# Kernel optimization log

Measured on AMD Instinct MI355X. Metric: run time of the kernel, lower is better.

Reference implementation:

```python
import jax, jax.numpy as jnp
import numpy as np

N, B = 16384, 64
NMC, RF = 4, 512
D0, D1, D2 = 1024, 512, 256
NATT, DATT = 4, 32


def _layer_norm(x, eps=1e-5):
    mu = jnp.mean(x, axis=-1, keepdims=True)
    var = jnp.var(x, axis=-1, keepdims=True)
    return (x - mu) / jnp.sqrt(var + eps)


def _rf_features(z):
    # rbf random features: concat(cos, sin) / sqrt(num_RF)
    scale = 1.0 / np.sqrt(z.shape[-1]).astype(np.float32)
    return jnp.concatenate([jnp.cos(z), jnp.sin(z)], axis=-1) * scale


def setup_inputs() -> dict:
    key = jax.random.key(0)
    ks = jax.random.split(key, 9)
    X = jax.random.normal(ks[0], (N, D0), dtype=jnp.float32)
    X_idx = jnp.sort(jax.random.randint(ks[1], (N,), 0, B, dtype=jnp.int32))
    Omega1 = jax.random.normal(ks[2], (NMC, D0, RF), dtype=jnp.float32) / np.sqrt(D0).astype(np.float32)
    Omega2 = jax.random.normal(ks[3], (NMC, D1, RF), dtype=jnp.float32) / np.sqrt(D1).astype(np.float32)
    W1 = jax.random.normal(ks[4], (2 * RF, D1), dtype=jnp.float32) * 0.02
    b1 = jnp.zeros((D1,), dtype=jnp.float32)
    W2 = jax.random.normal(ks[5], (2 * RF, D2), dtype=jnp.float32) * 0.02
    b2 = jnp.zeros((D2,), dtype=jnp.float32)
    Ws = jax.random.normal(ks[6], (D2, NATT), dtype=jnp.float32) * 0.02
    bs = jnp.zeros((NATT,), dtype=jnp.float32)
    Wm = jax.random.normal(ks[7], (D2, NATT * DATT), dtype=jnp.float32) * 0.02
    bm = jnp.zeros((NATT * DATT,), dtype=jnp.float32)
    return {"X": X, "X_idx": X_idx, "Omega1": Omega1, "Omega2": Omega2,
            "W1": W1, "b1": b1, "W2": W2, "b2": b2,
            "Ws": Ws, "bs": bs, "Wm": Wm, "bm": bm}


def reference(X, X_idx, Omega1, Omega2, W1, b1, W2, b2, Ws, bs, Wm, bm):
    # --- DGP_RF stack: two Omega(RF) + Linear blocks, MC-sampled Omegas ---
    z1 = jnp.einsum('nd,mdr->mnr', X, Omega1)            # [nMC, N, RF]
    phi1 = _layer_norm(_rf_features(z1))                  # [nMC, N, 2RF]
    h1 = jnp.einsum('mnf,fd->mnd', phi1, W1) + b1         # [nMC, N, D1]
    z2 = jnp.einsum('mnd,mdr->mnr', h1, Omega2)           # [nMC, N, RF]
    phi2 = _layer_norm(_rf_features(z2))                  # [nMC, N, 2RF]
    emb = jnp.einsum('mnf,fd->mnd', phi2, W2) + b2        # [nMC, N, D2]

    # --- Seed_Vecs: attention scores, segment softmax over instances ---
    scores = jnp.transpose(jnp.einsum('mnd,dk->mnk', emb, Ws) + bs, (1, 0, 2))  # [N, nMC, nAtt]
    probs = scores / np.sqrt(D2).astype(np.float32)
    seg = jax.ops.segment_sum(jnp.exp(probs), X_idx, num_segments=B)            # [B, nMC, nAtt]
    probs = jnp.exp(probs - jnp.log(seg)[X_idx])                                # segment softmax

    # --- MHa_Transform (default activation relu) + weighted segment pooling ---
    emb_new = jnp.transpose(jax.nn.relu(jnp.einsum('mnd,de->mne', emb, Wm) + bm), (1, 0, 2))  # [N, nMC, nAtt*dAtt]
    probs_rep = jnp.repeat(probs, DATT, axis=2)                                  # [N, nMC, nAtt*dAtt]
    embedds = jax.ops.segment_sum(emb_new * probs_rep, X_idx, num_segments=B)    # [B, nMC, nAtt*dAtt]
    return embedds
```

## Files before the change

kernel.cpp:

```cpp
#include <hip/hip_runtime.h>

#define NTOT 16384
#define NBAG 64
#define NMC  4

typedef __attribute__((ext_vector_type(8))) short bf8_t;
typedef __attribute__((ext_vector_type(4))) float f32x4;
typedef __attribute__((ext_vector_type(8))) unsigned short u16x8;

#define GLD16(g, l) __builtin_amdgcn_global_load_lds( \
    (const __attribute__((address_space(1))) void*)(g), \
    (__attribute__((address_space(3))) void*)(l), 16, 0, 0)

static __device__ __forceinline__ unsigned short f2bf(float x){
  unsigned int u = __float_as_uint(x);
  u += 0x7fffu + ((u >> 16) & 1u);
  return (unsigned short)(u >> 16);
}
static __device__ __forceinline__ float bf2f(unsigned short h){
  return __uint_as_float(((unsigned int)h) << 16);
}
static __device__ __forceinline__ f32x4 mfma16(bf8_t a, bf8_t b, f32x4 c){
  return __builtin_amdgcn_mfma_f32_16x16x32_bf16(a, b, c, 0, 0, 0);
}

__global__ __launch_bounds__(256) void k_cvt(const float* __restrict__ src,
    unsigned short* __restrict__ dst, int n8){
  for (int i = blockIdx.x*256 + threadIdx.x; i < n8; i += gridDim.x*256){
    float4 v0 = ((const float4*)src)[i*2];
    float4 v1 = ((const float4*)src)[i*2+1];
    u16x8 o;
    o[0]=f2bf(v0.x); o[1]=f2bf(v0.y); o[2]=f2bf(v0.z); o[3]=f2bf(v0.w);
    o[4]=f2bf(v1.x); o[5]=f2bf(v1.y); o[6]=f2bf(v1.z); o[7]=f2bf(v1.w);
    ((u16x8*)dst)[i] = o;
  }
}

__global__ __launch_bounds__(256) void k_pack8(const float* __restrict__ src,
    unsigned short* __restrict__ dst, int K, int N){
  const size_t base = (size_t)blockIdx.y * K * N;
  int idx = blockIdx.x*256 + threadIdx.x;
  int kg = idx / N, c = idx % N;
  const float* s = src + base + (size_t)(kg*8)*N + c;
  u16x8 o;
  #pragma unroll
  for (int i=0;i<8;i++) o[i] = f2bf(s[(size_t)i*N]);
  ((u16x8*)(dst + base))[idx] = o;
}

template<int RT>
static __device__ __forceinline__ void rf_ln_store(f32x4 (&acc)[RT][16],
    unsigned short* __restrict__ phiM, float* rowp, int row0,
    int n0, int ch, int l){
  const float scale = 0.044194173824159216f;
  const int g = l >> 4, li = l & 15;
  float part[RT][4];
  #pragma unroll
  for (int rt=0; rt<RT; rt++){
    #pragma unroll
    for (int j=0;j<4;j++){
      float s = 0.f;
      #pragma unroll
      for (int ct=0; ct<16; ct++){
        float sn, cs; __sincosf(acc[rt][ct][j], &sn, &cs);
        s += sn + cs;
      }
      #pragma unroll
      for (int off=1; off<16; off<<=1) s += __shfl_xor(s, off);
      part[rt][j] = s;
    }
  }
  __syncthreads();
  if (li == 0){
    #pragma unroll
    for (int rt=0; rt<RT; rt++)
      #pragma unroll
      for (int j=0;j<4;j++)
        rowp[(row0 + rt*16 + 4*g + j)*2 + ch] = part[rt][j];
  }
  __syncthreads();
  #pragma unroll
  for (int rt=0; rt<RT; rt++){
    #pragma unroll
    for (int j=0;j<4;j++){
      int rb = row0 + rt*16 + 4*g + j;
      float tot = rowp[rb*2+0] + rowp[rb*2+1];
      float mu = tot * (scale / 1024.0f);
      float rs = 1.0f / sqrtf((1.0f/1024.0f) - mu*mu + 1e-5f);
      size_t base = (size_t)(n0 + rb) * 1024;
      #pragma unroll
      for (int ct=0; ct<16; ct++){
        int c = ch*256 + ct*16 + li;
        float sn, cs; __sincosf(acc[rt][ct][j], &sn, &cs);
        phiM[base + c]       = f2bf((cs*scale - mu)*rs);
        phiM[base + 512 + c] = f2bf((sn*scale - mu)*rs);
      }
    }
  }
}


__global__ __launch_bounds__(512,2) void k_phi1(const unsigned short* __restrict__ Xb,
    const unsigned short* __restrict__ Om1f, unsigned short* __restrict__ phi){
  const int m = blockIdx.y, n0 = blockIdx.x*128;
  const int t = threadIdx.x, w = t>>6, l = t&63;
  const int g = l>>4, li = l&15;
  const int wrg = w>>1, ch = w&1;
  const int wvb = (t & ~63);
  __shared__ unsigned short Bs[4][16384];
  __shared__ float rowp[256];
  f32x4 acc[2][16];
  const f32x4 z4 = {0.f,0.f,0.f,0.f};
  #pragma unroll
  for (int rt=0;rt<2;rt++)
    #pragma unroll
    for (int ct=0;ct<16;ct++) acc[rt][ct] = z4;
  const unsigned short* bsrc = Om1f + (size_t)m*524288;
  const unsigned short* ar0 = Xb + (size_t)(n0 + wrg*32 + li)*1024 + g*8;
  const unsigned short* ar1 = ar0 + 16*1024;
  #pragma unroll
  for (int it=0; it<4; it++) GLD16(bsrc + it*4096 + t*8, &Bs[0][0] + it*4096 + wvb*8);
  #pragma unroll
  for (int it=0; it<4; it++) GLD16(bsrc + 16384 + it*4096 + t*8, &Bs[1][0] + it*4096 + wvb*8);
  bf8_t a0c = *(const bf8_t*)(ar0);       bf8_t a1c = *(const bf8_t*)(ar1);
  bf8_t a0n = *(const bf8_t*)(ar0 + 32);  bf8_t a1n = *(const bf8_t*)(ar1 + 32);
  for (int ks=0; ks<32; ks++){
    int ksn = ks+2 < 32 ? ks+2 : 31;
    const unsigned short* sb = bsrc + (size_t)ksn*16384;
    unsigned short* db = &Bs[(ks+2)&3][0];
    #pragma unroll
    for (int it=0; it<4; it++) GLD16(sb + it*4096 + t*8, db + it*4096 + wvb*8);
    bf8_t a0nn = *(const bf8_t*)(ar0 + ksn*32);
    bf8_t a1nn = *(const bf8_t*)(ar1 + ksn*32);
    asm volatile("s_waitcnt vmcnt(12)" ::: "memory");
    __builtin_amdgcn_sched_barrier(0);
    __builtin_amdgcn_s_barrier();
    __builtin_amdgcn_sched_barrier(0);
    const unsigned short* bb = &Bs[ks&3][0] + g*4096 + (ch*256)*8;
    __builtin_amdgcn_s_setprio(1);
    #pragma unroll
    for (int ct=0; ct<16; ct++){
      bf8_t b = *(const bf8_t*)(bb + (ct*16 + li)*8);
      acc[0][ct] = mfma16(a0c, b, acc[0][ct]);
      acc[1][ct] = mfma16(a1c, b, acc[1][ct]);
    }
    __builtin_amdgcn_s_setprio(0);
    a0c=a0n; a1c=a1n; a0n=a0nn; a1n=a1nn;
  }
  rf_ln_store<2>(acc, phi + (size_t)m*NTOT*1024, rowp, wrg*32, n0, ch, l);
}

__global__ __launch_bounds__(512,2) void k_phi2a(const unsigned short* __restrict__ phi,
    const unsigned short* __restrict__ W1f, const float* __restrict__ b1,
    unsigned short* __restrict__ h){
  const int m = blockIdx.y, n0 = blockIdx.x*128;
  const int t = threadIdx.x, w = t>>6, l = t&63;
  const int g = l>>4, li = l&15;
  const int wrg = w>>1, ch = w&1;
  const int wvb = (t & ~63);
  __shared__ unsigned short Bs[4][16384];
  f32x4 acc[2][16];
  const f32x4 z4 = {0.f,0.f,0.f,0.f};
  #pragma unroll
  for (int rt=0;rt<2;rt++)
    #pragma unroll
    for (int ct=0;ct<16;ct++) acc[rt][ct] = z4;
  const unsigned short* ar0 = phi + ((size_t)m*NTOT + n0 + wrg*32 + li)*1024 + g*8;
  const unsigned short* ar1 = ar0 + 16*1024;
  #pragma unroll
  for (int it=0; it<4; it++) GLD16(W1f + it*4096 + t*8, &Bs[0][0] + it*4096 + wvb*8);
  #pragma unroll
  for (int it=0; it<4; it++) GLD16(W1f + 16384 + it*4096 + t*8, &Bs[1][0] + it*4096 + wvb*8);
  bf8_t a0c = *(const bf8_t*)(ar0);       bf8_t a1c = *(const bf8_t*)(ar1);
  bf8_t a0n = *(const bf8_t*)(ar0 + 32);  bf8_t a1n = *(const bf8_t*)(ar1 + 32);
  for (int ks=0; ks<32; ks++){
    int ksn = ks+2 < 32 ? ks+2 : 31;
    const unsigned short* sb = W1f + (size_t)ksn*16384;
    unsigned short* db = &Bs[(ks+2)&3][0];
    #pragma unroll
    for (int it=0; it<4; it++) GLD16(sb + it*4096 + t*8, db + it*4096 + wvb*8);
    bf8_t a0nn = *(const bf8_t*)(ar0 + ksn*32);
    bf8_t a1nn = *(const bf8_t*)(ar1 + ksn*32);
    asm volatile("s_waitcnt vmcnt(12)" ::: "memory");
    __builtin_amdgcn_sched_barrier(0);
    __builtin_amdgcn_s_barrier();
    __builtin_amdgcn_sched_barrier(0);
    const unsigned short* bb = &Bs[ks&3][0] + g*4096 + (ch*256)*8;
    __builtin_amdgcn_s_setprio(1);
    #pragma unroll
    for (int ct=0; ct<16; ct++){
      bf8_t b = *(const bf8_t*)(bb + (ct*16 + li)*8);
      acc[0][ct] = mfma16(a0c, b, acc[0][ct]);
      acc[1][ct] = mfma16(a1c, b, acc[1][ct]);
    }
    __builtin_amdgcn_s_setprio(0);
    a0c=a0n; a1c=a1n; a0n=a0nn; a1n=a1nn;
  }
  #pragma unroll
  for (int rt=0; rt<2; rt++){
    #pragma unroll
    for (int ct=0; ct<16; ct++){
      int c = ch*256 + ct*16 + li;
      float bv = b1[c];
      #pragma unroll
      for (int j=0;j<4;j++)
        h[((size_t)m*NTOT + n0 + wrg*32 + rt*16 + 4*g + j)*512 + c] = f2bf(acc[rt][ct][j] + bv);
    }
  }
}

__global__ __launch_bounds__(512,2) void k_phi2b(const unsigned short* __restrict__ h,
    const unsigned short* __restrict__ Om2f, unsigned short* __restrict__ phi){
  const int m = blockIdx.y, n0 = blockIdx.x*128;
  const int t = threadIdx.x, w = t>>6, l = t&63;
  const int g = l>>4, li = l&15;
  const int wrg = w>>1, ch = w&1;
  const int wvb = (t & ~63);
  __shared__ unsigned short Bs[4][16384];
  __shared__ float rowp[256];
  f32x4 acc[2][16];
  const f32x4 z4 = {0.f,0.f,0.f,0.f};
  #pragma unroll
  for (int rt=0;rt<2;rt++)
    #pragma unroll
    for (int ct=0;ct<16;ct++) acc[rt][ct] = z4;
  const unsigned short* bsrc = Om2f + (size_t)m*262144;
  const unsigned short* ar0 = h + ((size_t)m*NTOT + n0 + wrg*32 + li)*512 + g*8;
  const unsigned short* ar1 = ar0 + 16*512;
  #pragma unroll
  for (int it=0; it<4; it++) GLD16(bsrc + it*4096 + t*8, &Bs[0][0] + it*4096 + wvb*8);
  #pragma unroll
  for (int it=0; it<4; it++) GLD16(bsrc + 16384 + it*4096 + t*8, &Bs[1][0] + it*4096 + wvb*8);
  bf8_t a0c = *(const bf8_t*)(ar0);       bf8_t a1c = *(const bf8_t*)(ar1);
  bf8_t a0n = *(const bf8_t*)(ar0 + 32);  bf8_t a1n = *(const bf8_t*)(ar1 + 32);
  for (int ks=0; ks<16; ks++){
    int ksn = ks+2 < 16 ? ks+2 : 15;
    const unsigned short* sb = bsrc + (size_t)ksn*16384;
    unsigned short* db = &Bs[(ks+2)&3][0];
    #pragma unroll
    for (int it=0; it<4; it++) GLD16(sb + it*4096 + t*8, db + it*4096 + wvb*8);
    bf8_t a0nn = *(const bf8_t*)(ar0 + ksn*32);
    bf8_t a1nn = *(const bf8_t*)(ar1 + ksn*32);
    asm volatile("s_waitcnt vmcnt(12)" ::: "memory");
    __builtin_amdgcn_sched_barrier(0);
    __builtin_amdgcn_s_barrier();
    __builtin_amdgcn_sched_barrier(0);
    const unsigned short* bb = &Bs[ks&3][0] + g*4096 + (ch*256)*8;
    __builtin_amdgcn_s_setprio(1);
    #pragma unroll
    for (int ct=0; ct<16; ct++){
      bf8_t b = *(const bf8_t*)(bb + (ct*16 + li)*8);
      acc[0][ct] = mfma16(a0c, b, acc[0][ct]);
      acc[1][ct] = mfma16(a1c, b, acc[1][ct]);
    }
    __builtin_amdgcn_s_setprio(0);
    a0c=a0n; a1c=a1n; a0n=a0nn; a1n=a1nn;
  }
  rf_ln_store<2>(acc, phi + (size_t)m*NTOT*1024, rowp, wrg*32, n0, ch, l);
}

__global__ __launch_bounds__(512,4) void k_emb(const unsigned short* __restrict__ phi,
    const unsigned short* __restrict__ W2f, const float* __restrict__ b2,
    unsigned short* __restrict__ emb){
  const int m = blockIdx.y, n0 = blockIdx.x*128;
  const int t = threadIdx.x, w = t>>6, l = t&63;
  const int g = l>>4, li = l&15;
  const int wvb = (t & ~63);
  __shared__ unsigned short Bs[4][8192];
  f32x4 acc[16];
  const f32x4 z4 = {0.f,0.f,0.f,0.f};
  #pragma unroll
  for (int ct=0;ct<16;ct++) acc[ct] = z4;
  const unsigned short* arow = phi + ((size_t)m*NTOT + n0 + w*16 + li)*1024 + g*8;
  #pragma unroll
  for (int it=0; it<2; it++) GLD16(W2f + it*4096 + t*8, &Bs[0][0] + it*4096 + wvb*8);
  #pragma unroll
  for (int it=0; it<2; it++) GLD16(W2f + 8192 + it*4096 + t*8, &Bs[1][0] + it*4096 + wvb*8);
  bf8_t ac = *(const bf8_t*)(arow);
  bf8_t an = *(const bf8_t*)(arow + 32);
  for (int ks=0; ks<32; ks++){
    int ksn = ks+2 < 32 ? ks+2 : 31;
    const unsigned short* sb = W2f + (size_t)ksn*8192;
    unsigned short* db = &Bs[(ks+2)&3][0];
    #pragma unroll
    for (int it=0; it<2; it++) GLD16(sb + it*4096 + t*8, db + it*4096 + wvb*8);
    bf8_t ann = *(const bf8_t*)(arow + ksn*32);
    asm volatile("s_waitcnt vmcnt(6)" ::: "memory");
    __builtin_amdgcn_sched_barrier(0);
    __builtin_amdgcn_s_barrier();
    __builtin_amdgcn_sched_barrier(0);
    const unsigned short* bb = &Bs[ks&3][0] + g*2048;
    __builtin_amdgcn_s_setprio(1);
    #pragma unroll
    for (int ct=0; ct<16; ct++){
      bf8_t b = *(const bf8_t*)(bb + (ct*16 + li)*8);
      acc[ct] = mfma16(ac, b, acc[ct]);
    }
    __builtin_amdgcn_s_setprio(0);
    ac = an; an = ann;
  }
  #pragma unroll
  for (int ct=0; ct<16; ct++){
    int c = ct*16 + li;
    float bv = b2[c];
    #pragma unroll
    for (int j=0;j<4;j++)
      emb[((size_t)m*NTOT + n0 + w*16 + 4*g + j)*256 + c] = f2bf(acc[ct][j] + bv);
  }
}

__global__ __launch_bounds__(256) void k_scores(const unsigned short* __restrict__ emb,
    const float* __restrict__ Wsm, const float* __restrict__ bsv, float* __restrict__ p){
  const int m = blockIdx.y;
  const int n = blockIdx.x*256 + threadIdx.x;
  __shared__ float Wss[1024];
  ((float4*)Wss)[threadIdx.x] = ((const float4*)Wsm)[threadIdx.x];
  __syncthreads();
  const u16x8* er = (const u16x8*)(emb + ((size_t)m*NTOT + n)*256);
  float a0=0.f,a1=0.f,a2=0.f,a3=0.f;
  for (int d8=0; d8<32; d8++){
    u16x8 e = er[d8];
    #pragma unroll
    for (int i=0;i<8;i++){
      float ev = bf2f(e[i]);
      const float* wv = &Wss[(d8*8+i)*4];
      a0 += ev*wv[0]; a1 += ev*wv[1]; a2 += ev*wv[2]; a3 += ev*wv[3];
    }
  }
  float4 o;
  o.x = expf((a0 + bsv[0]) * 0.0625f);
  o.y = expf((a1 + bsv[1]) * 0.0625f);
  o.z = expf((a2 + bsv[2]) * 0.0625f);
  o.w = expf((a3 + bsv[3]) * 0.0625f);
  ((float4*)p)[(size_t)m*NTOT + n] = o;
}

__global__ void k_starts(const int* __restrict__ idx, int* __restrict__ starts){
  int t = threadIdx.x;
  if (t <= NBAG){
    int lo = 0, hi = NTOT;
    while (lo < hi){ int mid = (lo + hi) >> 1; if (idx[mid] < t) lo = mid + 1; else hi = mid; }
    starts[t] = lo;
  }
}

__global__ __launch_bounds__(256) void k_embnew(const unsigned short* __restrict__ emb,
    const unsigned short* __restrict__ Wmf, const float* __restrict__ bm,
    unsigned short* __restrict__ en){
  const int m = blockIdx.y, n0 = blockIdx.x*64;
  const int t = threadIdx.x, w = t>>6, l = t&63;
  const int g = l>>4, li = l&15;
  const int wvb = (t & ~63);
  __shared__ unsigned short Bs[32768];
  #pragma unroll
  for (int it=0; it<16; it++)
    GLD16(Wmf + it*2048 + t*8, Bs + it*2048 + wvb*8);
  asm volatile("s_waitcnt vmcnt(0)" ::: "memory");
  __syncthreads();
  f32x4 acc[8];
  const f32x4 z4 = {0.f,0.f,0.f,0.f};
  #pragma unroll
  for (int ct=0;ct<8;ct++) acc[ct] = z4;
  const unsigned short* arow = emb + ((size_t)m*NTOT + n0 + w*16 + li)*256 + g*8;
  #pragma unroll
  for (int ks=0; ks<8; ks++){
    bf8_t a = *(const bf8_t*)(arow + ks*32);
    #pragma unroll
    for (int ct=0; ct<8; ct++){
      bf8_t b = *(const bf8_t*)(Bs + (ks*4+g)*1024 + (ct*16 + li)*8);
      acc[ct] = mfma16(a, b, acc[ct]);
    }
  }
  #pragma unroll
  for (int ct=0; ct<8; ct++){
    int c = ct*16 + li;
    float bv = bm[c];
    #pragma unroll
    for (int j=0;j<4;j++)
      en[((size_t)m*NTOT + n0 + w*16 + 4*g + j)*128 + c] = f2bf(fmaxf(acc[ct][j] + bv, 0.f));
  }
}

__global__ __launch_bounds__(256) void k_pool(const unsigned short* __restrict__ en,
    const float* __restrict__ p, const int* __restrict__ starts, float* __restrict__ out){
  const int b = blockIdx.x, m = blockIdx.y;
  const int t = threadIdx.x;
  const int s0 = starts[b], s1 = starts[b+1];
  float sp0=0.f,sp1=0.f,sp2=0.f,sp3=0.f;
  for (int n = s0 + t; n < s1; n += 256){
    float4 pv = ((const float4*)p)[(size_t)m*NTOT + n];
    sp0 += pv.x; sp1 += pv.y; sp2 += pv.z; sp3 += pv.w;
  }
  #pragma unroll
  for (int off=1; off<64; off<<=1){
    sp0 += __shfl_xor(sp0, off); sp1 += __shfl_xor(sp1, off);
    sp2 += __shfl_xor(sp2, off); sp3 += __shfl_xor(sp3, off);
  }
  __shared__ float wred[4][4];
  __shared__ float winv[4];
  if ((t & 63) == 0){ wred[t>>6][0]=sp0; wred[t>>6][1]=sp1; wred[t>>6][2]=sp2; wred[t>>6][3]=sp3; }
  __syncthreads();
  if (t < 4){
    float s = wred[0][t] + wred[1][t] + wred[2][t] + wred[3][t];
    winv[t] = (s > 0.f) ? 1.0f / s : 0.f;
  }
  __syncthreads();
  const int e = t & 127, half = t >> 7;
  const int k = e >> 5;
  float accv = 0.f;
  for (int n = s0 + half; n < s1; n += 2){
    float wq = p[((size_t)m*NTOT + n)*4 + k];
    float v = bf2f(en[((size_t)m*NTOT + n)*128 + e]);
    accv = fmaf(v, wq, accv);
  }
  accv *= winv[k];
  __shared__ float ac2[2][128];
  ac2[half][e] = accv;
  __syncthreads();
  if (t < 128) out[((size_t)b*NMC + m)*128 + t] = ac2[0][t] + ac2[1][t];
}

extern "C" void kernel_launch(void* const* d_in, const int* in_sizes, int n_in,
                              void* d_out, int out_size, void* d_ws, size_t ws_size,
                              hipStream_t stream) {
  const float* X    = (const float*)d_in[0];
  const int*   Xidx = (const int*)  d_in[1];
  const float* Om1  = (const float*)d_in[2];
  const float* Om2  = (const float*)d_in[3];
  const float* W1   = (const float*)d_in[4];
  const float* b1   = (const float*)d_in[5];
  const float* W2   = (const float*)d_in[6];
  const float* b2   = (const float*)d_in[7];
  const float* Wsm  = (const float*)d_in[8];
  const float* bsv  = (const float*)d_in[9];
  const float* Wm   = (const float*)d_in[10];
  const float* bm   = (const float*)d_in[11];
  float* out = (float*)d_out;

  char* ws = (char*)d_ws;
  unsigned short* phi  = (unsigned short*)(ws);
  unsigned short* en   = (unsigned short*)(ws);
  float* p             = (float*)(ws + 16777216ull);
  int* starts          = (int*)(ws + 17825792ull);
  unsigned short* h    = (unsigned short*)(ws + 134217728ull);
  unsigned short* Xb   = (unsigned short*)(ws + 134217728ull);
  unsigned short* emb  = (unsigned short*)(ws + 134217728ull);
  unsigned short* Om1f = (unsigned short*)(ws + 201326592ull);
  unsigned short* W1f  = (unsigned short*)(ws + 205520896ull);
  unsigned short* Om2f = (unsigned short*)(ws + 206569472ull);
  unsigned short* W2f  = (unsigned short*)(ws + 208666624ull);
  unsigned short* Wmf  = (unsigned short*)(ws + 209190912ull);

  k_cvt   <<<2048, 256, 0, stream>>>(X, Xb, NTOT*1024/8);
  k_pack8 <<<dim3(256,4), 256, 0, stream>>>(Om1, Om1f, 1024, 512);
  k_pack8 <<<dim3(256,1), 256, 0, stream>>>(W1,  W1f,  1024, 512);
  k_pack8 <<<dim3(128,4), 256, 0, stream>>>(Om2, Om2f, 512,  512);
  k_pack8 <<<dim3(128,1), 256, 0, stream>>>(W2,  W2f,  1024, 256);
  k_pack8 <<<dim3(16,1),  256, 0, stream>>>(Wm,  Wmf,  256,  128);
  k_phi1  <<<dim3(128,4), 512, 0, stream>>>(Xb, Om1f, phi);
  k_phi2a <<<dim3(128,4), 512, 0, stream>>>(phi, W1f, b1, h);
  k_phi2b <<<dim3(128,4), 512, 0, stream>>>(h, Om2f, phi);
  k_emb   <<<dim3(128,4), 512, 0, stream>>>(phi, W2f, b2, emb);
  k_scores<<<dim3(64,4),  256, 0, stream>>>(emb, Wsm, bsv, p);
  k_embnew<<<dim3(256,4), 256, 0, stream>>>(emb, Wmf, bm, en);
  k_starts<<<1, 128, 0, stream>>>(Xidx, starts);
  k_pool  <<<dim3(64,4),  256, 0, stream>>>(en, p, starts, out);
}
```

Measured before the change: 530.5 us.

## Retile GEMM warps to 2x4 row/column grid with 64x128 per-warp tiles

```diff
diff --git a/kernel.cpp b/kernel.cpp
--- a/kernel.cpp
+++ b/kernel.cpp
@@ -48,20 +48,20 @@
   ((u16x8*)(dst + base))[idx] = o;
 }
 
-template<int RT>
-static __device__ __forceinline__ void rf_ln_store(f32x4 (&acc)[RT][16],
-    unsigned short* __restrict__ phiM, float* rowp, int row0,
-    int n0, int ch, int l){
+static __device__ __forceinline__ void rf_ln_store4(f32x4 (&acc)[4][8],
+    unsigned short* __restrict__ phiM, float* rowp, int rowg,
+    int n0, int colg, int l){
   const float scale = 0.044194173824159216f;
   const int g = l >> 4, li = l & 15;
-  float part[RT][4];
-  #pragma unroll
-  for (int rt=0; rt<RT; rt++){
+  const int row0 = rowg*64;
+  float part[4][4];
+  #pragma unroll
+  for (int rt=0; rt<4; rt++){
     #pragma unroll
     for (int j=0;j<4;j++){
       float s = 0.f;
       #pragma unroll
-      for (int ct=0; ct<16; ct++){
+      for (int ct=0; ct<8; ct++){
         float sn, cs; __sincosf(acc[rt][ct][j], &sn, &cs);
         s += sn + cs;
       }
@@ -70,27 +70,26 @@
       part[rt][j] = s;
     }
   }
-  __syncthreads();
   if (li == 0){
     #pragma unroll
-    for (int rt=0; rt<RT; rt++)
+    for (int rt=0; rt<4; rt++)
       #pragma unroll
       for (int j=0;j<4;j++)
-        rowp[(row0 + rt*16 + 4*g + j)*2 + ch] = part[rt][j];
-  }
-  __syncthreads();
-  #pragma unroll
-  for (int rt=0; rt<RT; rt++){
+        rowp[(row0 + rt*16 + 4*g + j)*4 + colg] = part[rt][j];
+  }
+  __syncthreads();
+  #pragma unroll
+  for (int rt=0; rt<4; rt++){
     #pragma unroll
     for (int j=0;j<4;j++){
       int rb = row0 + rt*16 + 4*g + j;
-      float tot = rowp[rb*2+0] + rowp[rb*2+1];
+      float tot = rowp[rb*4+0] + rowp[rb*4+1] + rowp[rb*4+2] + rowp[rb*4+3];
       float mu = tot * (scale / 1024.0f);
       float rs = 1.0f / sqrtf((1.0f/1024.0f) - mu*mu + 1e-5f);
       size_t base = (size_t)(n0 + rb) * 1024;
       #pragma unroll
-      for (int ct=0; ct<16; ct++){
-        int c = ch*256 + ct*16 + li;
+      for (int ct=0; ct<8; ct++){
+        int c = colg*128 + ct*16 + li;
         float sn, cs; __sincosf(acc[rt][ct][j], &sn, &cs);
         phiM[base + c]       = f2bf((cs*scale - mu)*rs);
         phiM[base + 512 + c] = f2bf((sn*scale - mu)*rs);
@@ -105,49 +104,53 @@
   const int m = blockIdx.y, n0 = blockIdx.x*128;
   const int t = threadIdx.x, w = t>>6, l = t&63;
   const int g = l>>4, li = l&15;
-  const int wrg = w>>1, ch = w&1;
-  const int wvb = (t & ~63);
+  const int rowg = w & 1, colg = w >> 1;
+  const int wvb = t & ~63;
   __shared__ unsigned short Bs[4][16384];
-  __shared__ float rowp[256];
-  f32x4 acc[2][16];
+  __shared__ float rowp[512];
+  f32x4 acc[4][8];
   const f32x4 z4 = {0.f,0.f,0.f,0.f};
   #pragma unroll
-  for (int rt=0;rt<2;rt++)
-    #pragma unroll
-    for (int ct=0;ct<16;ct++) acc[rt][ct] = z4;
+  for (int rt=0;rt<4;rt++)
+    #pragma unroll
+    for (int ct=0;ct<8;ct++) acc[rt][ct] = z4;
   const unsigned short* bsrc = Om1f + (size_t)m*524288;
-  const unsigned short* ar0 = Xb + (size_t)(n0 + wrg*32 + li)*1024 + g*8;
-  const unsigned short* ar1 = ar0 + 16*1024;
+  const unsigned short* abase = Xb + (size_t)(n0 + rowg*64 + li)*1024 + g*8;
+  bf8_t a_c[4], a_n[4];
   #pragma unroll
   for (int it=0; it<4; it++) GLD16(bsrc + it*4096 + t*8, &Bs[0][0] + it*4096 + wvb*8);
   #pragma unroll
+  for (int rt=0; rt<4; rt++) a_c[rt] = *(const bf8_t*)(abase + rt*16384);
+  #pragma unroll
   for (int it=0; it<4; it++) GLD16(bsrc + 16384 + it*4096 + t*8, &Bs[1][0] + it*4096 + wvb*8);
-  bf8_t a0c = *(const bf8_t*)(ar0);       bf8_t a1c = *(const bf8_t*)(ar1);
-  bf8_t a0n = *(const bf8_t*)(ar0 + 32);  bf8_t a1n = *(const bf8_t*)(ar1 + 32);
+  #pragma unroll
+  for (int rt=0; rt<4; rt++) a_n[rt] = *(const bf8_t*)(abase + rt*16384 + 32);
   for (int ks=0; ks<32; ks++){
     int ksn = ks+2 < 32 ? ks+2 : 31;
     const unsigned short* sb = bsrc + (size_t)ksn*16384;
     unsigned short* db = &Bs[(ks+2)&3][0];
     #pragma unroll
     for (int it=0; it<4; it++) GLD16(sb + it*4096 + t*8, db + it*4096 + wvb*8);
-    bf8_t a0nn = *(const bf8_t*)(ar0 + ksn*32);
-    bf8_t a1nn = *(const bf8_t*)(ar1 + ksn*32);
-    asm volatile("s_waitcnt vmcnt(12)" ::: "memory");
+    bf8_t a_nn[4];
+    #pragma unroll
+    for (int rt=0; rt<4; rt++) a_nn[rt] = *(const bf8_t*)(abase + rt*16384 + ksn*32);
+    asm volatile("s_waitcnt vmcnt(16)" ::: "memory");
     __builtin_amdgcn_sched_barrier(0);
     __builtin_amdgcn_s_barrier();
     __builtin_amdgcn_sched_barrier(0);
-    const unsigned short* bb = &Bs[ks&3][0] + g*4096 + (ch*256)*8;
+    const unsigned short* bb = &Bs[ks&3][0] + g*4096 + (colg*128 + li)*8;
     __builtin_amdgcn_s_setprio(1);
     #pragma unroll
-    for (int ct=0; ct<16; ct++){
-      bf8_t b = *(const bf8_t*)(bb + (ct*16 + li)*8);
-      acc[0][ct] = mfma16(a0c, b, acc[0][ct]);
-      acc[1][ct] = mfma16(a1c, b, acc[1][ct]);
+    for (int ct=0; ct<8; ct++){
+      bf8_t b = *(const bf8_t*)(bb + ct*128);
+      #pragma unroll
+      for (int rt=0; rt<4; rt++) acc[rt][ct] = mfma16(a_c[rt], b, acc[rt][ct]);
     }
     __builtin_amdgcn_s_setprio(0);
-    a0c=a0n; a1c=a1n; a0n=a0nn; a1n=a1nn;
-  }
-  rf_ln_store<2>(acc, phi + (size_t)m*NTOT*1024, rowp, wrg*32, n0, ch, l);
+    #pragma unroll
+    for (int rt=0; rt<4; rt++){ a_c[rt]=a_n[rt]; a_n[rt]=a_nn[rt]; }
+  }
+  rf_ln_store4(acc, phi + (size_t)m*NTOT*1024, rowp, rowg, n0, colg, l);
 }
 
 __global__ __launch_bounds__(512,2) void k_phi2a(const unsigned short* __restrict__ phi,
@@ -156,55 +159,59 @@
   const int m = blockIdx.y, n0 = blockIdx.x*128;
   const int t = threadIdx.x, w = t>>6, l = t&63;
   const int g = l>>4, li = l&15;
-  const int wrg = w>>1, ch = w&1;
-  const int wvb = (t & ~63);
+  const int rowg = w & 1, colg = w >> 1;
+  const int wvb = t & ~63;
   __shared__ unsigned short Bs[4][16384];
-  f32x4 acc[2][16];
+  f32x4 acc[4][8];
   const f32x4 z4 = {0.f,0.f,0.f,0.f};
   #pragma unroll
-  for (int rt=0;rt<2;rt++)
-    #pragma unroll
-    for (int ct=0;ct<16;ct++) acc[rt][ct] = z4;
-  const unsigned short* ar0 = phi + ((size_t)m*NTOT + n0 + wrg*32 + li)*1024 + g*8;
-  const unsigned short* ar1 = ar0 + 16*1024;
+  for (int rt=0;rt<4;rt++)
+    #pragma unroll
+    for (int ct=0;ct<8;ct++) acc[rt][ct] = z4;
+  const unsigned short* abase = phi + ((size_t)m*NTOT + n0 + rowg*64 + li)*1024 + g*8;
+  bf8_t a_c[4], a_n[4];
   #pragma unroll
   for (int it=0; it<4; it++) GLD16(W1f + it*4096 + t*8, &Bs[0][0] + it*4096 + wvb*8);
   #pragma unroll
+  for (int rt=0; rt<4; rt++) a_c[rt] = *(const bf8_t*)(abase + rt*16384);
+  #pragma unroll
   for (int it=0; it<4; it++) GLD16(W1f + 16384 + it*4096 + t*8, &Bs[1][0] + it*4096 + wvb*8);
-  bf8_t a0c = *(const bf8_t*)(ar0);       bf8_t a1c = *(const bf8_t*)(ar1);
-  bf8_t a0n = *(const bf8_t*)(ar0 + 32);  bf8_t a1n = *(const bf8_t*)(ar1 + 32);
+  #pragma unroll
+  for (int rt=0; rt<4; rt++) a_n[rt] = *(const bf8_t*)(abase + rt*16384 + 32);
   for (int ks=0; ks<32; ks++){
     int ksn = ks+2 < 32 ? ks+2 : 31;
     const unsigned short* sb = W1f + (size_t)ksn*16384;
     unsigned short* db = &Bs[(ks+2)&3][0];
     #pragma unroll
     for (int it=0; it<4; it++) GLD16(sb + it*4096 + t*8, db + it*4096 + wvb*8);
-    bf8_t a0nn = *(const bf8_t*)(ar0 + ksn*32);
-    bf8_t a1nn = *(const bf8_t*)(ar1 + ksn*32);
-    asm volatile("s_waitcnt vmcnt(12)" ::: "memory");
+    bf8_t a_nn[4];
+    #pragma unroll
+    for (int rt=0; rt<4; rt++) a_nn[rt] = *(const bf8_t*)(abase + rt*16384 + ksn*32);
+    asm volatile("s_waitcnt vmcnt(16)" ::: "memory");
     __builtin_amdgcn_sched_barrier(0);
     __builtin_amdgcn_s_barrier();
     __builtin_amdgcn_sched_barrier(0);
-    const unsigned short* bb = &Bs[ks&3][0] + g*4096 + (ch*256)*8;
+    const unsigned short* bb = &Bs[ks&3][0] + g*4096 + (colg*128 + li)*8;
     __builtin_amdgcn_s_setprio(1);
     #pragma unroll
-    for (int ct=0; ct<16; ct++){
-      bf8_t b = *(const bf8_t*)(bb + (ct*16 + li)*8);
-      acc[0][ct] = mfma16(a0c, b, acc[0][ct]);
-      acc[1][ct] = mfma16(a1c, b, acc[1][ct]);
+    for (int ct=0; ct<8; ct++){
+      bf8_t b = *(const bf8_t*)(bb + ct*128);
+      #pragma unroll
+      for (int rt=0; rt<4; rt++) acc[rt][ct] = mfma16(a_c[rt], b, acc[rt][ct]);
     }
     __builtin_amdgcn_s_setprio(0);
-    a0c=a0n; a1c=a1n; a0n=a0nn; a1n=a1nn;
-  }
-  #pragma unroll
-  for (int rt=0; rt<2; rt++){
-    #pragma unroll
-    for (int ct=0; ct<16; ct++){
-      int c = ch*256 + ct*16 + li;
+    #pragma unroll
+    for (int rt=0; rt<4; rt++){ a_c[rt]=a_n[rt]; a_n[rt]=a_nn[rt]; }
+  }
+  #pragma unroll
+  for (int rt=0; rt<4; rt++){
+    #pragma unroll
+    for (int ct=0; ct<8; ct++){
+      int c = colg*128 + ct*16 + li;
       float bv = b1[c];
       #pragma unroll
       for (int j=0;j<4;j++)
-        h[((size_t)m*NTOT + n0 + wrg*32 + rt*16 + 4*g + j)*512 + c] = f2bf(acc[rt][ct][j] + bv);
+        h[((size_t)m*NTOT + n0 + rowg*64 + rt*16 + 4*g + j)*512 + c] = f2bf(acc[rt][ct][j] + bv);
     }
   }
 }
@@ -214,98 +221,115 @@
   const int m = blockIdx.y, n0 = blockIdx.x*128;
   const int t = threadIdx.x, w = t>>6, l = t&63;
   const int g = l>>4, li = l&15;
-  const int wrg = w>>1, ch = w&1;
-  const int wvb = (t & ~63);
+  const int rowg = w & 1, colg = w >> 1;
+  const int wvb = t & ~63;
   __shared__ unsigned short Bs[4][16384];
-  __shared__ float rowp[256];
-  f32x4 acc[2][16];
+  __shared__ float rowp[512];
+  f32x4 acc[4][8];
   const f32x4 z4 = {0.f,0.f,0.f,0.f};
   #pragma unroll
-  for (int rt=0;rt<2;rt++)
-    #pragma unroll
-    for (int ct=0;ct<16;ct++) acc[rt][ct] = z4;
+  for (int rt=0;rt<4;rt++)
+    #pragma unroll
+    for (int ct=0;ct<8;ct++) acc[rt][ct] = z4;
   const unsigned short* bsrc = Om2f + (size_t)m*262144;
-  const unsigned short* ar0 = h + ((size_t)m*NTOT + n0 + wrg*32 + li)*512 + g*8;
-  const unsigned short* ar1 = ar0 + 16*512;
+  const unsigned short* abase = h + ((size_t)m*NTOT + n0 + rowg*64 + li)*512 + g*8;
+  bf8_t a_c[4], a_n[4];
   #pragma unroll
   for (int it=0; it<4; it++) GLD16(bsrc + it*4096 + t*8, &Bs[0][0] + it*4096 + wvb*8);
   #pragma unroll
+  for (int rt=0; rt<4; rt++) a_c[rt] = *(const bf8_t*)(abase + rt*8192);
+  #pragma unroll
   for (int it=0; it<4; it++) GLD16(bsrc + 16384 + it*4096 + t*8, &Bs[1][0] + it*4096 + wvb*8);
-  bf8_t a0c = *(const bf8_t*)(ar0);       bf8_t a1c = *(const bf8_t*)(ar1);
-  bf8_t a0n = *(const bf8_t*)(ar0 + 32);  bf8_t a1n = *(const bf8_t*)(ar1 + 32);
+  #pragma unroll
+  for (int rt=0; rt<4; rt++) a_n[rt] = *(const bf8_t*)(abase + rt*8192 + 32);
   for (int ks=0; ks<16; ks++){
     int ksn = ks+2 < 16 ? ks+2 : 15;
     const unsigned short* sb = bsrc + (size_t)ksn*16384;
     unsigned short* db = &Bs[(ks+2)&3][0];
     #pragma unroll
     for (int it=0; it<4; it++) GLD16(sb + it*4096 + t*8, db + it*4096 + wvb*8);
-    bf8_t a0nn = *(const bf8_t*)(ar0 + ksn*32);
-    bf8_t a1nn = *(const bf8_t*)(ar1 + ksn*32);
-    asm volatile("s_waitcnt vmcnt(12)" ::: "memory");
+    bf8_t a_nn[4];
+    #pragma unroll
+    for (int rt=0; rt<4; rt++) a_nn[rt] = *(const bf8_t*)(abase + rt*8192 + ksn*32);
+    asm volatile("s_waitcnt vmcnt(16)" ::: "memory");
     __builtin_amdgcn_sched_barrier(0);
     __builtin_amdgcn_s_barrier();
     __builtin_amdgcn_sched_barrier(0);
-    const unsigned short* bb = &Bs[ks&3][0] + g*4096 + (ch*256)*8;
+    const unsigned short* bb = &Bs[ks&3][0] + g*4096 + (colg*128 + li)*8;
     __builtin_amdgcn_s_setprio(1);
     #pragma unroll
-    for (int ct=0; ct<16; ct++){
-      bf8_t b = *(const bf8_t*)(bb + (ct*16 + li)*8);
-      acc[0][ct] = mfma16(a0c, b, acc[0][ct]);
-      acc[1][ct] = mfma16(a1c, b, acc[1][ct]);
+    for (int ct=0; ct<8; ct++){
+      bf8_t b = *(const bf8_t*)(bb + ct*128);
+      #pragma unroll
+      for (int rt=0; rt<4; rt++) acc[rt][ct] = mfma16(a_c[rt], b, acc[rt][ct]);
     }
     __builtin_amdgcn_s_setprio(0);
-    a0c=a0n; a1c=a1n; a0n=a0nn; a1n=a1nn;
-  }
-  rf_ln_store<2>(acc, phi + (size_t)m*NTOT*1024, rowp, wrg*32, n0, ch, l);
-}
-
-__global__ __launch_bounds__(512,4) void k_emb(const unsigned short* __restrict__ phi,
+    #pragma unroll
+    for (int rt=0; rt<4; rt++){ a_c[rt]=a_n[rt]; a_n[rt]=a_nn[rt]; }
+  }
+  rf_ln_store4(acc, phi + (size_t)m*NTOT*1024, rowp, rowg, n0, colg, l);
+}
+
+__global__ __launch_bounds__(512,2) void k_emb(const unsigned short* __restrict__ phi,
     const unsigned short* __restrict__ W2f, const float* __restrict__ b2,
     unsigned short* __restrict__ emb){
   const int m = blockIdx.y, n0 = blockIdx.x*128;
   const int t = threadIdx.x, w = t>>6, l = t&63;
   const int g = l>>4, li = l&15;
-  const int wvb = (t & ~63);
+  const int rowg = w & 1, colg = w >> 1;
+  const int wvb = t & ~63;
   __shared__ unsigned short Bs[4][8192];
-  f32x4 acc[16];
+  f32x4 acc[4][4];
   const f32x4 z4 = {0.f,0.f,0.f,0.f};
   #pragma unroll
-  for (int ct=0;ct<16;ct++) acc[ct] = z4;
-  const unsigned short* arow = phi + ((size_t)m*NTOT + n0 + w*16 + li)*1024 + g*8;
+  for (int rt=0;rt<4;rt++)
+    #pragma unroll
+    for (int ct=0;ct<4;ct++) acc[rt][ct] = z4;
+  const unsigned short* abase = phi + ((size_t)m*NTOT + n0 + rowg*64 + li)*1024 + g*8;
+  bf8_t a_c[4], a_n[4];
   #pragma unroll
   for (int it=0; it<2; it++) GLD16(W2f + it*4096 + t*8, &Bs[0][0] + it*4096 + wvb*8);
   #pragma unroll
+  for (int rt=0; rt<4; rt++) a_c[rt] = *(const bf8_t*)(abase + rt*16384);
+  #pragma unroll
   for (int it=0; it<2; it++) GLD16(W2f + 8192 + it*4096 + t*8, &Bs[1][0] + it*4096 + wvb*8);
-  bf8_t ac = *(const bf8_t*)(arow);
-  bf8_t an = *(const bf8_t*)(arow + 32);
+  #pragma unroll
+  for (int rt=0; rt<4; rt++) a_n[rt] = *(const bf8_t*)(abase + rt*16384 + 32);
   for (int ks=0; ks<32; ks++){
     int ksn = ks+2 < 32 ? ks+2 : 31;
     const unsigned short* sb = W2f + (size_t)ksn*8192;
     unsigned short* db = &Bs[(ks+2)&3][0];
     #pragma unroll
     for (int it=0; it<2; it++) GLD16(sb + it*4096 + t*8, db + it*4096 + wvb*8);
-    bf8_t ann = *(const bf8_t*)(arow + ksn*32);
-    asm volatile("s_waitcnt vmcnt(6)" ::: "memory");
+    bf8_t a_nn[4];
+    #pragma unroll
+    for (int rt=0; rt<4; rt++) a_nn[rt] = *(const bf8_t*)(abase + rt*16384 + ksn*32);
+    asm volatile("s_waitcnt vmcnt(12)" ::: "memory");
     __builtin_amdgcn_sched_barrier(0);
     __builtin_amdgcn_s_barrier();
     __builtin_amdgcn_sched_barrier(0);
-    const unsigned short* bb = &Bs[ks&3][0] + g*2048;
+    const unsigned short* bb = &Bs[ks&3][0] + g*2048 + (colg*64 + li)*8;
     __builtin_amdgcn_s_setprio(1);
     #pragma unroll
-    for (int ct=0; ct<16; ct++){
-      bf8_t b = *(const bf8_t*)(bb + (ct*16 + li)*8);
-      acc[ct] = mfma16(ac, b, acc[ct]);
+    for (int ct=0; ct<4; ct++){
+      bf8_t b = *(const bf8_t*)(bb + ct*128);
+      #pragma unroll
+      for (int rt=0; rt<4; rt++) acc[rt][ct] = mfma16(a_c[rt], b, acc[rt][ct]);
     }
     __builtin_amdgcn_s_setprio(0);
-    ac = an; an = ann;
-  }
-  #pragma unroll
-  for (int ct=0; ct<16; ct++){
-    int c = ct*16 + li;
-    float bv = b2[c];
-    #pragma unroll
-    for (int j=0;j<4;j++)
-      emb[((size_t)m*NTOT + n0 + w*16 + 4*g + j)*256 + c] = f2bf(acc[ct][j] + bv);
+    #pragma unroll
+    for (int rt=0; rt<4; rt++){ a_c[rt]=a_n[rt]; a_n[rt]=a_nn[rt]; }
+  }
+  #pragma unroll
+  for (int rt=0; rt<4; rt++){
+    #pragma unroll
+    for (int ct=0; ct<4; ct++){
+      int c = colg*64 + ct*16 + li;
+      float bv = b2[c];
+      #pragma unroll
+      for (int j=0;j<4;j++)
+        emb[((size_t)m*NTOT + n0 + rowg*64 + rt*16 + 4*g + j)*256 + c] = f2bf(acc[rt][ct][j] + bv);
+    }
   }
 }
 
```

New measurement: 614.2 us. +15.8%, slower.
